# Optimization experiments

Hardware: AMD Instinct MI355X
Metric: run time of the kernel (lower is better)

Reference implementation:

```python
import jax, jax.numpy as jnp
import numpy as np

DEPTH = 4
DIM = 768
HEADS = 12
DH = 64
INNER = HEADS * DH            # 768
FF_INNER = int(4 * (2.0 / 3.0) * DIM)  # 2048 (GEGLU paper sizing)
B, N = 4, 1024                # N must be a perfect square (2D rotary)
ATTN_SCALE = 8.0              # cosine-sim attention scale from Attention(scale=8)
EPS = 1e-5


def _ln(x, gamma, beta):
    mu = jnp.mean(x, axis=-1, keepdims=True)
    var = jnp.mean((x - mu) ** 2, axis=-1, keepdims=True)
    return (x - mu) * jax.lax.rsqrt(var + EPS) * gamma + beta


def _rope_angles(n, dh):
    # precompute_freqs_cis_2d: x/y positions on sqrt(n) grid, dh//4 freqs each, interleaved
    H = int(n ** 0.5)
    pos = jnp.arange(n)
    xp = (pos % H).astype(jnp.float32)
    yp = (pos // H).astype(jnp.float32)
    freqs = 1.0 / (10000.0 ** (jnp.arange(0, dh, 4)[: dh // 4].astype(jnp.float32) / dh))
    xa = jnp.outer(xp, freqs)  # [n, dh//4]
    ya = jnp.outer(yp, freqs)
    return jnp.stack([xa, ya], axis=-1).reshape(n, dh // 2)  # [n, dh//2]


def _apply_rope(t, cos, sin):
    # t: [B, N, H, DH]; complex-pair rotation on last dim
    tr = t.reshape(*t.shape[:-1], DH // 2, 2)
    r, im = tr[..., 0], tr[..., 1]
    c = cos[None, :, None, :]
    s = sin[None, :, None, :]
    out = jnp.stack([r * c - im * s, r * s + im * c], axis=-1)
    return out.reshape(t.shape)


def _l2norm(t):
    return t / jnp.maximum(jnp.linalg.norm(t, axis=-1, keepdims=True), 1e-12)


def setup_inputs() -> dict:
    key = jax.random.key(0)
    ks = jax.random.split(key, 10)
    w = 0.02
    return {
        "x": jax.random.normal(ks[0], (B, N, DIM), dtype=jnp.float32),
        "attn_gamma": jnp.ones((DEPTH, DIM), dtype=jnp.float32),
        "wq": w * jax.random.normal(ks[1], (DEPTH, DIM, INNER), dtype=jnp.float32),
        "wkv": w * jax.random.normal(ks[2], (DEPTH, DIM, 2 * INNER), dtype=jnp.float32),
        "q_scale": jnp.ones((DEPTH, DH), dtype=jnp.float32),
        "k_scale": jnp.ones((DEPTH, DH), dtype=jnp.float32),
        "wo": w * jax.random.normal(ks[3], (DEPTH, INNER, DIM), dtype=jnp.float32),
        "ff_gamma": jnp.ones((DEPTH, DIM), dtype=jnp.float32),
        "ff_beta": jnp.zeros((DEPTH, DIM), dtype=jnp.float32),
        "wff1": w * jax.random.normal(ks[4], (DEPTH, DIM, 2 * FF_INNER), dtype=jnp.float32),
        "wff2": w * jax.random.normal(ks[5], (DEPTH, FF_INNER, DIM), dtype=jnp.float32),
    }


def reference(x, attn_gamma, wq, wkv, q_scale, k_scale, wo, ff_gamma, ff_beta, wff1, wff2):
    b, n, _ = x.shape
    ang = _rope_angles(n, DH)
    cos, sin = jnp.cos(ang), jnp.sin(ang)
    for i in range(DEPTH):
        # ---- Attention (qk-l2norm cosine attention, 2D rotary, scale=8) ----
        h = _ln(x, attn_gamma[i], 0.0)          # Attention.norm (beta is a zero buffer)
        kv_in = x                                # faithful: kv_input taken BEFORE norm
        q = (h @ wq[i]).reshape(b, n, HEADS, DH)
        kv = kv_in @ wkv[i]
        k, v = jnp.split(kv, 2, axis=-1)
        k = k.reshape(b, n, HEADS, DH)
        v = v.reshape(b, n, HEADS, DH)
        q = _apply_rope(q, cos, sin)
        k = _apply_rope(k, cos, sin)
        q = jnp.transpose(q, (0, 2, 1, 3))       # b h n d
        k = jnp.transpose(k, (0, 2, 1, 3))
        v = jnp.transpose(v, (0, 2, 1, 3))
        q = _l2norm(q) * q_scale[i]
        k = _l2norm(k) * k_scale[i]
        sim = jnp.einsum('bhid,bhjd->bhij', q, k) * ATTN_SCALE
        attn = jax.nn.softmax(sim, axis=-1)
        o = jnp.einsum('bhij,bhjd->bhid', attn, v)
        o = jnp.transpose(o, (0, 2, 1, 3)).reshape(b, n, INNER)
        x = x + o @ wo[i]
        # ---- GEGLU FeedForward ----
        hf = _ln(x, ff_gamma[i], ff_beta[i])
        u = hf @ wff1[i]
        a, g = jnp.split(u, 2, axis=-1)
        x = x + (a * jax.nn.gelu(g, approximate=False)) @ wff2[i]
    return x
```

## Files before the change

kernel.cpp:

```cpp
#include <hip/hip_runtime.h>
#include <hip/hip_bf16.h>
#include <math.h>

typedef __hip_bfloat16 bf16;
typedef __bf16 bf16x8 __attribute__((ext_vector_type(8)));
typedef float f32x4 __attribute__((ext_vector_type(4)));

#define NDEPTH 4
#define DIM 768
#define HEADS 12
#define DH 64
#define INNER 768
#define FFI 2048
#define BB 4
#define NN 1024
#define ROWS (BB*NN)

__device__ __forceinline__ void async_cp16(const bf16* g, bf16* l) {
  __builtin_amdgcn_global_load_lds(
      (const __attribute__((address_space(1))) unsigned int*)g,
      (__attribute__((address_space(3))) unsigned int*)l, 16, 0, 0);
}

template<int BN, bool GELU, bool VOUT, int K, int LD>
__device__ __forceinline__ void gemm_body(
    const bf16* __restrict__ A, const bf16* __restrict__ Bt,
    bf16* __restrict__ Cb, float* __restrict__ Cf, const float* __restrict__ Rf,
    bf16* __restrict__ Vt, int M, int N, int bx, int by, bf16* As, bf16* Bs)
{
  constexpr int WN = BN / 2;
  constexpr int NT = WN / 16;
  const int tid  = threadIdx.x;
  const int lane = tid & 63, w = tid >> 6;
  const int quad = lane >> 4, l16 = lane & 15;
  const int wr = w >> 1, wc = w & 1;
  const int m0 = by * 128, n0 = bx * BN;

  f32x4 acc[4][NT] = {};

  constexpr int CHA = 128 * 8;
  constexpr int CH  = CHA + BN * 8;
  constexpr int NCH = CH / 256;
  constexpr int NTK = K / 64;

  auto stage = [&](int kk, int buf) {
    bf16* Asb = As + buf * (128*64);
    bf16* Bsb = Bs + buf * (BN*64);
    #pragma unroll
    for (int t = 0; t < NCH; ++t) {
      int c0 = w*64 + t*256;
      int ch = c0 + lane;
      if (c0 < CHA) {
        int r = ch >> 3, j = (ch & 7) ^ (r & 7);
        async_cp16(&A[(size_t)(m0 + r)*LD + kk + j*8], &Asb[(size_t)c0*8]);
      } else {
        int ch2 = ch - CHA, r = ch2 >> 3, j = (ch2 & 7) ^ (r & 7);
        async_cp16(&Bt[(size_t)(n0 + r)*LD + kk + j*8], &Bsb[(size_t)(c0 - CHA)*8]);
      }
    }
  };

  stage(0, 0);
  __syncthreads();

  #pragma unroll
  for (int t = 0; t < NTK; ++t) {
    const int buf = t & 1;
    if (t + 1 < NTK) stage((t + 1) * 64, buf ^ 1);

    const bf16* Asb = As + buf * (128*64);
    const bf16* Bsb = Bs + buf * (BN*64);

    #pragma unroll
    for (int kc = 0; kc < 2; ++kc) {
      bf16x8 bfr[NT];
      #pragma unroll
      for (int nt = 0; nt < NT; ++nt) {
        int rb = wc*WN + nt*16 + l16;
        int c  = (kc*4 + quad) ^ (rb & 7);
        bfr[nt] = *(const bf16x8*)&Bsb[rb*64 + c*8];
      }
      #pragma unroll
      for (int mt = 0; mt < 4; ++mt) {
        int ra = wr*64 + mt*16 + l16;
        int ca = (kc*4 + quad) ^ (ra & 7);
        bf16x8 af = *(const bf16x8*)&Asb[ra*64 + ca*8];
        #pragma unroll
        for (int nt = 0; nt < NT; ++nt)
          acc[mt][nt] = __builtin_amdgcn_mfma_f32_16x16x32_bf16(af, bfr[nt], acc[mt][nt], 0, 0, 0);
      }
    }
    if (t + 1 < NTK) __syncthreads();
  }

  #pragma unroll
  for (int mt = 0; mt < 4; ++mt) {
    #pragma unroll
    for (int nt = 0; nt < NT; ++nt) {
      int row = m0 + wr*64 + mt*16 + quad*4;
      int col = n0 + wc*WN + nt*16 + l16;
      if (GELU) {
        #pragma unroll
        for (int r = 0; r < 4; ++r) {
          float v = acc[mt][nt][r];
          float g = __shfl_xor(v, 1);
          if (!(lane & 1)) {
            float ge = 0.5f * g * (1.f + erff(g * 0.70710678118654752f));
            Cb[(size_t)(row + r)*(N >> 1) + (col >> 1)] = __float2bfloat16(v * ge);
          }
        }
      } else if (VOUT) {
        if (col < INNER) {
          #pragma unroll
          for (int r = 0; r < 4; ++r)
            Cb[(size_t)(row + r)*INNER + col] = __float2bfloat16(acc[mt][nt][r]);
        } else {
          int c2 = col - INNER, hh = c2 >> 6, d = c2 & 63;
          int b = row >> 10, nn = row & 1023;
          union { ushort4 u4; bf16 h4[4]; } p;
          #pragma unroll
          for (int r = 0; r < 4; ++r) p.h4[r] = __float2bfloat16(acc[mt][nt][r]);
          *(ushort4*)&Vt[(((size_t)b*HEADS + hh)*DH + d)*NN + nn] = p.u4;
        }
      } else {
        #pragma unroll
        for (int r = 0; r < 4; ++r) {
          float v = acc[mt][nt][r];
          size_t idx = (size_t)(row + r) * N + col;
          if (Rf) v += Rf[idx];
          if (Cf) Cf[idx] = v;
          if (Cb) Cb[idx] = __float2bfloat16(v);
        }
      }
    }
  }
}

template<int BN, int KH, int LD>
__global__ __launch_bounds__(256) void gemm_splitk_kernel(
    const bf16* __restrict__ A, const bf16* __restrict__ Bt,
    float* __restrict__ P, int M, int N)
{
  __shared__ __align__(16) bf16 As[2*128*64];
  __shared__ __align__(16) bf16 Bs[2*BN*64];
  const int z = blockIdx.z;
  gemm_body<BN,false,false,KH,LD>(A + (size_t)z*KH, Bt + (size_t)z*KH, nullptr,
                                  P + (size_t)z*M*N, nullptr, nullptr,
                                  M, N, blockIdx.x, blockIdx.y, As, Bs);
}

__global__ __launch_bounds__(256) void qkv_kernel(
    const bf16* __restrict__ h, const bf16* __restrict__ x16,
    const bf16* __restrict__ wqT, const bf16* __restrict__ wkvT,
    bf16* __restrict__ qb, bf16* __restrict__ kb, bf16* __restrict__ vt)
{
  __shared__ __align__(16) bf16 As[2*128*64];
  __shared__ __align__(16) bf16 Bs[2*128*64];
  if (blockIdx.z == 0)
    gemm_body<64,false,false,768,768>(h, wqT, qb, nullptr, nullptr, nullptr,
                                      ROWS, INNER, blockIdx.x, blockIdx.y, As, Bs);
  else
    gemm_body<128,false,true,768,768>(x16, wkvT, kb, nullptr, nullptr, vt,
                                      ROWS, 2*INNER, blockIdx.x, blockIdx.y, As, Bs);
}

__global__ __launch_bounds__(512) void gemm256_kernel(
    const bf16* __restrict__ A, const bf16* __restrict__ Bt,
    bf16* __restrict__ Cb, int M, int N)
{
  __shared__ __align__(16) bf16 As[2][256*64];
  __shared__ __align__(16) bf16 Bs[2][256*64];

  const int tid  = threadIdx.x;
  const int lane = tid & 63, wv = tid >> 6;
  const int quad = lane >> 4, l16 = lane & 15;
  const int wr = wv >> 2, wc = wv & 3;

  const int lin = blockIdx.y * gridDim.x + blockIdx.x;
  const int xcd = lin & 7, loc = lin >> 3;
  const int bxs = (xcd & 1) * 8 + (loc & 7);
  const int bys = (xcd >> 1) * 4 + (loc >> 3);
  const int m0 = bys * 256, n0 = bxs * 256;

  f32x4 acc[8][4] = {};

  auto stage = [&](int kk, int buf) {
    #pragma unroll
    for (int t = 0; t < 8; ++t) {
      int c0 = wv*64 + t*512;
      int ch = c0 + lane;
      if (c0 < 2048) {
        int r = ch >> 3, j = (ch & 7) ^ (r & 7);
        async_cp16(&A[(size_t)(m0 + r)*768 + kk + j*8], &As[buf][(size_t)c0*8]);
      } else {
        int ch2 = ch - 2048, r = ch2 >> 3, j = (ch2 & 7) ^ (r & 7);
        async_cp16(&Bt[(size_t)(n0 + r)*768 + kk + j*8], &Bs[buf][(size_t)(c0 - 2048)*8]);
      }
    }
  };

  stage(0, 0);
  __syncthreads();

  #pragma unroll
  for (int t = 0; t < 12; ++t) {
    const int buf = t & 1;
    if (t + 1 < 12) stage((t + 1) * 64, buf ^ 1);

    const bf16* Asb = &As[buf][0];
    const bf16* Bsb = &Bs[buf][0];

    #pragma unroll
    for (int kc = 0; kc < 2; ++kc) {
      bf16x8 bfr[4];
      #pragma unroll
      for (int nt = 0; nt < 4; ++nt) {
        int rb = wc*64 + nt*16 + l16;
        int c  = (kc*4 + quad) ^ (rb & 7);
        bfr[nt] = *(const bf16x8*)&Bsb[rb*64 + c*8];
      }
      #pragma unroll
      for (int mt = 0; mt < 8; ++mt) {
        int ra = wr*128 + mt*16 + l16;
        int ca = (kc*4 + quad) ^ (ra & 7);
        bf16x8 af = *(const bf16x8*)&Asb[ra*64 + ca*8];
        #pragma unroll
        for (int nt = 0; nt < 4; ++nt)
          acc[mt][nt] = __builtin_amdgcn_mfma_f32_16x16x32_bf16(af, bfr[nt], acc[mt][nt], 0, 0, 0);
      }
    }
    if (t + 1 < 12) __syncthreads();
  }

  #pragma unroll
  for (int mt = 0; mt < 8; ++mt) {
    #pragma unroll
    for (int nt = 0; nt < 4; ++nt) {
      int row = m0 + wr*128 + mt*16 + quad*4;
      int col = n0 + wc*64 + nt*16 + l16;
      #pragma unroll
      for (int r = 0; r < 4; ++r) {
        float v = acc[mt][nt][r];
        float g = __shfl_xor(v, 1);
        if (!(lane & 1)) {
          float ge = 0.5f * g * (1.f + erff(g * 0.70710678118654752f));
          Cb[(size_t)(row + r)*(N >> 1) + (col >> 1)] = __float2bfloat16(v * ge);
        }
      }
    }
  }
}

__global__ __launch_bounds__(256) void ln_kernel(
    const float* __restrict__ x, const float* __restrict__ g,
    const float* __restrict__ bta, bf16* __restrict__ out)
{
  const int row = blockIdx.x, tid = threadIdx.x;
  const size_t base = (size_t)row * DIM;
  float v[3];
  #pragma unroll
  for (int j = 0; j < 3; ++j) v[j] = x[base + tid + j*256];
  float s  = v[0] + v[1] + v[2];
  float ss = v[0]*v[0] + v[1]*v[1] + v[2]*v[2];
  #pragma unroll
  for (int off = 32; off; off >>= 1) { s += __shfl_xor(s, off); ss += __shfl_xor(ss, off); }
  __shared__ float red[8];
  int w = tid >> 6;
  if ((tid & 63) == 0) { red[w] = s; red[w + 4] = ss; }
  __syncthreads();
  s  = red[0] + red[1] + red[2] + red[3];
  ss = red[4] + red[5] + red[6] + red[7];
  float mean = s * (1.f/768.f);
  float var  = ss * (1.f/768.f) - mean*mean;
  float rstd = rsqrtf(fmaxf(var, 0.f) + 1e-5f);
  #pragma unroll
  for (int j = 0; j < 3; ++j) {
    int c = tid + j*256;
    float bv = bta ? bta[c] : 0.f;
    out[base + c] = __float2bfloat16((v[j] - mean) * rstd * g[c] + bv);
  }
}

__global__ __launch_bounds__(256) void redln_kernel(
    const float* __restrict__ P0, const float* __restrict__ P1,
    const float* __restrict__ res,
    float* __restrict__ xo32, bf16* __restrict__ xo16, float* __restrict__ outf,
    const float* __restrict__ g, const float* __restrict__ bta,
    bf16* __restrict__ lnout)
{
  const int row = blockIdx.x, tid = threadIdx.x;
  const size_t base = (size_t)row * DIM;
  float v[3];
  #pragma unroll
  for (int j = 0; j < 3; ++j) {
    size_t idx = base + tid + j*256;
    v[j] = res[idx] + P0[idx] + P1[idx];
    if (xo32) xo32[idx] = v[j];
    if (xo16) xo16[idx] = __float2bfloat16(v[j]);
    if (outf) outf[idx] = v[j];
  }
  if (!g) return;
  float s  = v[0] + v[1] + v[2];
  float ss = v[0]*v[0] + v[1]*v[1] + v[2]*v[2];
  #pragma unroll
  for (int off = 32; off; off >>= 1) { s += __shfl_xor(s, off); ss += __shfl_xor(ss, off); }
  __shared__ float red[8];
  int w = tid >> 6;
  if ((tid & 63) == 0) { red[w] = s; red[w + 4] = ss; }
  __syncthreads();
  s  = red[0] + red[1] + red[2] + red[3];
  ss = red[4] + red[5] + red[6] + red[7];
  float mean = s * (1.f/768.f);
  float var  = ss * (1.f/768.f) - mean*mean;
  float rstd = rsqrtf(fmaxf(var, 0.f) + 1e-5f);
  #pragma unroll
  for (int j = 0; j < 3; ++j) {
    int c = tid + j*256;
    float bv = bta ? bta[c] : 0.f;
    lnout[base + c] = __float2bfloat16((v[j] - mean) * rstd * g[c] + bv);
  }
}

__global__ __launch_bounds__(384) void rope_kernel(
    const bf16* __restrict__ q, const bf16* __restrict__ kb,
    const float* __restrict__ qsc, const float* __restrict__ ksc,
    bf16* __restrict__ qh, bf16* __restrict__ kh)
{
  const int bn = blockIdx.x;
  const int b = bn >> 10, n = bn & 1023;
  const int tid = threadIdx.x;
  const int h = tid >> 5, pr = tid & 31, d0 = pr*2;
  const float xp = (float)(n & 31), yp = (float)(n >> 5);
  const int t = pr >> 1;
  const float freq = powf(10000.f, -(float)t / 16.f);
  const float ang = (pr & 1) ? yp * freq : xp * freq;
  float sn, cs;
  sincosf(ang, &sn, &cs);
  const float2 qs2 = *(const float2*)&qsc[d0];
  const float2 ks2 = *(const float2*)&ksc[d0];

  union { unsigned int u; bf16 h2[2]; } qa, ka, qo, ko;
  qa.u = *(const unsigned int*)&q [(size_t)bn*INNER + h*64 + d0];
  ka.u = *(const unsigned int*)&kb[(size_t)bn*INNER + h*64 + d0];
  float qre = __bfloat162float(qa.h2[0]), qim = __bfloat162float(qa.h2[1]);
  float kre = __bfloat162float(ka.h2[0]), kim = __bfloat162float(ka.h2[1]);
  float qr = qre*cs - qim*sn, qi = qre*sn + qim*cs;
  float kr = kre*cs - kim*sn, ki = kre*sn + kim*cs;
  float q2 = qr*qr + qi*qi, k2 = kr*kr + ki*ki;
  #pragma unroll
  for (int off = 1; off < 32; off <<= 1) { q2 += __shfl_xor(q2, off); k2 += __shfl_xor(k2, off); }
  float qinv = 8.f / fmaxf(sqrtf(q2), 1e-12f);
  float kinv = 1.f / fmaxf(sqrtf(k2), 1e-12f);
  qo.h2[0] = __float2bfloat16(qr * qinv * qs2.x);
  qo.h2[1] = __float2bfloat16(qi * qinv * qs2.y);
  ko.h2[0] = __float2bfloat16(kr * kinv * ks2.x);
  ko.h2[1] = __float2bfloat16(ki * kinv * ks2.y);
  size_t oi = (((size_t)b*HEADS + h)*NN + n)*DH + d0;
  *(unsigned int*)&qh[oi] = qo.u;
  *(unsigned int*)&kh[oi] = ko.u;
}

__global__ __launch_bounds__(256) void attn_kernel(
    const bf16* __restrict__ qh, const bf16* __restrict__ kh,
    const bf16* __restrict__ vt, const float* __restrict__ qsc,
    const float* __restrict__ ksc, bf16* __restrict__ ob)
{
  __shared__ __align__(16) bf16 Qs[64*64];
  __shared__ __align__(16) bf16 Ks[2][64*64];
  __shared__ __align__(16) bf16 Vs[2][64*64];
  __shared__ __align__(16) bf16 Ps[4][16*72];

  const int tid = threadIdx.x;
  const int lane = tid & 63, w = tid >> 6;
  const int quad = lane >> 4, l16 = lane & 15;
  const int qt = blockIdx.x, bh = blockIdx.y;
  const int b = bh / HEADS, h = bh % HEADS;
  const size_t base = (size_t)bh * NN * DH;

  float mq = fabsf(qsc[lane]), mk = fabsf(ksc[lane]);
  #pragma unroll
  for (int off = 1; off < 64; off <<= 1) {
    mq = fmaxf(mq, __shfl_xor(mq, off));
    mk = fmaxf(mk, __shfl_xor(mk, off));
  }
  const float Mb = 8.f * mq * mk;

  #pragma unroll
  for (int t = 0; t < 2; ++t) {
    int c0 = w*64 + t*256, ch = c0 + lane;
    int r = ch >> 3, jl = (ch & 7) ^ (r & 7);
    async_cp16(&qh[base + (size_t)(qt*64 + r)*64 + jl*8], &Qs[(size_t)c0*8]);
  }

  auto stage_kv = [&](int kt0, int buf) {
    #pragma unroll
    for (int t = 0; t < 4; ++t) {
      int c0 = w*64 + t*256, ch = c0 + lane;
      if (c0 < 512) {
        int r = ch >> 3, jl = (ch & 7) ^ (r & 7);
        async_cp16(&kh[base + (size_t)(kt0*64 + r)*64 + jl*8],
                   &Ks[buf][(size_t)c0*8]);
      } else {
        int ch2 = ch - 512, r = ch2 >> 3, jl = (ch2 & 7) ^ (r & 7);
        async_cp16(&vt[base + (size_t)r*NN + kt0*64 + jl*8],
                   &Vs[buf][(size_t)(c0 - 512)*8]);
      }
    }
  };

  f32x4 o[4] = {};
  float pl[4] = {0.f, 0.f, 0.f, 0.f};

  stage_kv(0, 0);
  __syncthreads();

  for (int kt0 = 0; kt0 < NN/64; ++kt0) {
    const int buf = kt0 & 1;
    if (kt0 + 1 < NN/64) stage_kv(kt0 + 1, buf ^ 1);

    f32x4 s[4] = {};
    bf16x8 aq[2];
    const int rq = w*16 + l16;
    #pragma unroll
    for (int kc = 0; kc < 2; ++kc)
      aq[kc] = *(const bf16x8*)&Qs[rq*64 + ((kc*4 + quad) ^ (rq & 7))*8];
    #pragma unroll
    for (int kt = 0; kt < 4; ++kt)
      #pragma unroll
      for (int kc = 0; kc < 2; ++kc) {
        int rb = kt*16 + l16;
        bf16x8 bk = *(const bf16x8*)&Ks[buf][rb*64 + ((kc*4 + quad) ^ (rb & 7))*8];
        s[kt] = __builtin_amdgcn_mfma_f32_16x16x32_bf16(aq[kc], bk, s[kt], 0, 0, 0);
      }

    #pragma unroll
    for (int r = 0; r < 4; ++r) {
      #pragma unroll
      for (int kt = 0; kt < 4; ++kt) {
        float pv = __expf(s[kt][r] - Mb);
        pl[r] += pv;
        Ps[w][(quad*4 + r)*72 + kt*16 + l16] = __float2bfloat16(pv);
      }
    }

    #pragma unroll
    for (int kc = 0; kc < 2; ++kc) {
      bf16x8 ap = *(const bf16x8*)&Ps[w][l16*72 + kc*32 + quad*8];
      #pragma unroll
      for (int nt = 0; nt < 4; ++nt) {
        int rv = nt*16 + l16;
        bf16x8 bv = *(const bf16x8*)&Vs[buf][rv*64 + ((kc*4 + quad) ^ (rv & 7))*8];
        o[nt] = __builtin_amdgcn_mfma_f32_16x16x32_bf16(ap, bv, o[nt], 0, 0, 0);
      }
    }

    if (kt0 + 1 < NN/64) __syncthreads();
  }

  float l[4];
  #pragma unroll
  for (int r = 0; r < 4; ++r) {
    float rs = pl[r];
    #pragma unroll
    for (int off = 1; off < 16; off <<= 1) rs += __shfl_xor(rs, off);
    l[r] = rs;
  }

  #pragma unroll
  for (int nt = 0; nt < 4; ++nt)
    #pragma unroll
    for (int r = 0; r < 4; ++r) {
      int n = qt*64 + w*16 + quad*4 + r;
      int dcol = nt*16 + l16;
      ob[((size_t)(b*NN + n)*HEADS + h)*DH + dcol] = __float2bfloat16(o[nt][r] / l[r]);
    }
}

__global__ __launch_bounds__(256) void cast_kernel(
    const float* __restrict__ x, bf16* __restrict__ o)
{
  size_t i = ((size_t)blockIdx.x*256 + threadIdx.x) * 8;
  float4 f0 = *(const float4*)(x + i);
  float4 f1 = *(const float4*)(x + i + 4);
  union { uint4 u; bf16 h[8]; } p;
  p.h[0] = __float2bfloat16(f0.x); p.h[1] = __float2bfloat16(f0.y);
  p.h[2] = __float2bfloat16(f0.z); p.h[3] = __float2bfloat16(f0.w);
  p.h[4] = __float2bfloat16(f1.x); p.h[5] = __float2bfloat16(f1.y);
  p.h[6] = __float2bfloat16(f1.z); p.h[7] = __float2bfloat16(f1.w);
  *(uint4*)(o + i) = p.u;
}

struct TD { const float* src; bf16* dst; int R, C, base, perm; };
struct TDs5 { TD d[5]; };

__global__ __launch_bounds__(256) void wtrans_kernel(TDs5 a)
{
  const int blk = blockIdx.x;
  int di = 0;
  #pragma unroll
  for (int k = 1; k < 5; ++k) if (blk >= a.d[k].base) di = k;
  const TD d = a.d[di];
  const int local = blk - d.base;
  const int tilesX = d.C >> 5;
  const int by = local / tilesX, bx = local - by*tilesX;
  __shared__ float t[32][33];
  const int tx = threadIdx.x & 31, ty = threadIdx.x >> 5;
  const int c0 = bx*32, r0 = by*32;
  #pragma unroll
  for (int i = 0; i < 4; ++i)
    t[ty + i*8][tx] = d.src[(size_t)(r0 + ty + i*8)*d.C + c0 + tx];
  __syncthreads();
  const int half = d.C >> 1;
  #pragma unroll
  for (int i = 0; i < 4; ++i) {
    int c = c0 + ty + i*8;
    int rout = d.perm ? ((c < half) ? 2*c : 2*(c - half) + 1) : c;
    d.dst[(size_t)rout*d.R + r0 + tx] = __float2bfloat16(t[tx][ty + i*8]);
  }
}

extern "C" void kernel_launch(void* const* d_in, const int* in_sizes, int n_in,
                              void* d_out, int out_size, void* d_ws, size_t ws_size,
                              hipStream_t stream)
{
  const float* x_in       = (const float*)d_in[0];
  const float* attn_gamma = (const float*)d_in[1];
  const float* wq         = (const float*)d_in[2];
  const float* wkv        = (const float*)d_in[3];
  const float* q_scale    = (const float*)d_in[4];
  const float* k_scale    = (const float*)d_in[5];
  const float* wo         = (const float*)d_in[6];
  const float* ff_gamma   = (const float*)d_in[7];
  const float* ff_beta    = (const float*)d_in[8];
  const float* wff1       = (const float*)d_in[9];
  const float* wff2       = (const float*)d_in[10];
  float* outp = (float*)d_out;
  char* ws = (char*)d_ws;

  const size_t E = (size_t)ROWS * DIM;
  float* xw32 = (float*)ws;
  bf16*  xw16 = (bf16*)(ws + 12582912);
  bf16*  S_h  = (bf16*)(ws + 18874368);
  char*  BIGb = ws + 25165824;
  bf16*  WT   = (bf16*)(ws + 62914560);
  bf16*  qbuf  = (bf16*)BIGb;
  bf16*  kbuf  = qbuf + E;
  bf16*  qhb   = qbuf + 2*E;
  bf16*  khb   = qbuf + 3*E;
  bf16*  vtb   = qbuf + 4*E;
  bf16*  glbuf = (bf16*)BIGb;
  float* wP    = (float*)BIGb;
  float* fP    = (float*)(BIGb + 16777216);
  bf16*  wqT   = WT;
  bf16*  wkvT  = WT + 589824;
  bf16*  woT   = WT + 1769472;
  bf16*  wff1T = WT + 2359296;
  bf16*  wff2T = WT + 5505024;

  cast_kernel<<<1536, 256, 0, stream>>>(x_in, xw16);
  ln_kernel<<<ROWS, 256, 0, stream>>>(x_in, attn_gamma, nullptr, S_h);

  for (int i = 0; i < NDEPTH; ++i) {
    const float* xsrc = (i == 0) ? x_in : xw32;

    TDs5 td;
    td.d[0] = { wq   + (size_t)i*589824,  wqT,   768,  768,    0, 0 };
    td.d[1] = { wkv  + (size_t)i*1179648, wkvT,  768, 1536,  576, 0 };
    td.d[2] = { wo   + (size_t)i*589824,  woT,   768,  768, 1728, 0 };
    td.d[3] = { wff1 + (size_t)i*3145728, wff1T, 768, 4096, 2304, 1 };
    td.d[4] = { wff2 + (size_t)i*1572864, wff2T, 2048, 768, 5376, 0 };
    wtrans_kernel<<<6912, 256, 0, stream>>>(td);

    qkv_kernel<<<dim3(12,32,2), 256, 0, stream>>>(S_h, xw16, wqT, wkvT, qbuf, kbuf, vtb);
    rope_kernel<<<ROWS, 384, 0, stream>>>(qbuf, kbuf, q_scale + i*DH, k_scale + i*DH, qhb, khb);
    attn_kernel<<<dim3(16,48), 256, 0, stream>>>(qhb, khb, vtb,
                                                 q_scale + i*DH, k_scale + i*DH, S_h);
    gemm_splitk_kernel<64,384,768><<<dim3(12,32,2), 256, 0, stream>>>(S_h, woT, wP, ROWS, DIM);
    redln_kernel<<<ROWS, 256, 0, stream>>>(wP, wP + E, xsrc, xw32, nullptr, nullptr,
                                           ff_gamma + i*DIM, ff_beta + i*DIM, S_h);
    gemm256_kernel<<<dim3(16,16), 512, 0, stream>>>(S_h, wff1T, glbuf, ROWS, 2*FFI);
    gemm_splitk_kernel<64,1024,2048><<<dim3(12,32,2), 256, 0, stream>>>(glbuf, wff2T, fP, ROWS, DIM);
    if (i < NDEPTH-1)
      redln_kernel<<<ROWS, 256, 0, stream>>>(fP, fP + E, xw32, xw32, xw16, nullptr,
                                             attn_gamma + (i+1)*DIM, nullptr, S_h);
    else
      redln_kernel<<<ROWS, 256, 0, stream>>>(fP, fP + E, xw32, nullptr, nullptr, outp,
                                             nullptr, nullptr, nullptr);
  }
}
```

Measured before the change: 907.9 us.

## Split 256x256 GEGLU GEMM K-tiles into half-stages with fine-grained async pipelining

Restructures the FF1 GEGLU GEMM main loop so each 64-wide K tile is split into two 32-wide halves with separate LDS buffers. Loads for A and B halves are issued interleaved with four MFMA phases, using partial vmcnt waits, raw s_barrier and s_setprio around MFMA bursts. The aim is to overlap global-to-LDS copies with matrix math more finely and cut full-tile barrier stalls. It adds manual waitcnt bookkeeping that must match the number of outstanding loads, which is fragile.

```diff
diff --git a/kernel.cpp b/kernel.cpp
--- a/kernel.cpp
+++ b/kernel.cpp
@@ -168,8 +168,8 @@
     const bf16* __restrict__ A, const bf16* __restrict__ Bt,
     bf16* __restrict__ Cb, int M, int N)
 {
-  __shared__ __align__(16) bf16 As[2][256*64];
-  __shared__ __align__(16) bf16 Bs[2][256*64];
+  __shared__ __align__(16) bf16 As[2][2][256*32];
+  __shared__ __align__(16) bf16 Bs[2][2][256*32];
 
   const int tid  = threadIdx.x;
   const int lane = tid & 63, wv = tid >> 6;
@@ -184,52 +184,96 @@
 
   f32x4 acc[8][4] = {};
 
-  auto stage = [&](int kk, int buf) {
-    #pragma unroll
-    for (int t = 0; t < 8; ++t) {
+  auto stage_half = [&](const bf16* __restrict__ G, int row0, int colbase,
+                        bf16* L) {
+    #pragma unroll
+    for (int t = 0; t < 2; ++t) {
       int c0 = wv*64 + t*512;
       int ch = c0 + lane;
-      if (c0 < 2048) {
-        int r = ch >> 3, j = (ch & 7) ^ (r & 7);
-        async_cp16(&A[(size_t)(m0 + r)*768 + kk + j*8], &As[buf][(size_t)c0*8]);
-      } else {
-        int ch2 = ch - 2048, r = ch2 >> 3, j = (ch2 & 7) ^ (r & 7);
-        async_cp16(&Bt[(size_t)(n0 + r)*768 + kk + j*8], &Bs[buf][(size_t)(c0 - 2048)*8]);
-      }
+      int r = ch >> 2, jsw = ch & 3, jh = jsw ^ (r & 3);
+      async_cp16(&G[(size_t)(row0 + r)*768 + colbase + jh*8],
+                 &L[(size_t)c0*8]);
     }
   };
 
-  stage(0, 0);
-  __syncthreads();
-
-  #pragma unroll
-  for (int t = 0; t < 12; ++t) {
-    const int buf = t & 1;
-    if (t + 1 < 12) stage((t + 1) * 64, buf ^ 1);
-
-    const bf16* Asb = &As[buf][0];
-    const bf16* Bsb = &Bs[buf][0];
-
-    #pragma unroll
-    for (int kc = 0; kc < 2; ++kc) {
-      bf16x8 bfr[4];
-      #pragma unroll
-      for (int nt = 0; nt < 4; ++nt) {
-        int rb = wc*64 + nt*16 + l16;
-        int c  = (kc*4 + quad) ^ (rb & 7);
-        bfr[nt] = *(const bf16x8*)&Bsb[rb*64 + c*8];
-      }
-      #pragma unroll
-      for (int mt = 0; mt < 8; ++mt) {
-        int ra = wr*128 + mt*16 + l16;
-        int ca = (kc*4 + quad) ^ (ra & 7);
-        bf16x8 af = *(const bf16x8*)&Asb[ra*64 + ca*8];
-        #pragma unroll
-        for (int nt = 0; nt < 4; ++nt)
-          acc[mt][nt] = __builtin_amdgcn_mfma_f32_16x16x32_bf16(af, bfr[nt], acc[mt][nt], 0, 0, 0);
-      }
-    }
-    if (t + 1 < 12) __syncthreads();
+  auto rdA = [&](const bf16* Ab, bf16x8* af) {
+    #pragma unroll
+    for (int mt = 0; mt < 8; ++mt) {
+      int ra = wr*128 + mt*16 + l16;
+      af[mt] = *(const bf16x8*)&Ab[ra*32 + (quad ^ (ra & 3))*8];
+    }
+  };
+  auto rdB = [&](const bf16* Bb, int ntg, bf16x8* bfr) {
+    #pragma unroll
+    for (int i = 0; i < 2; ++i) {
+      int rb = wc*64 + (ntg*2 + i)*16 + l16;
+      bfr[i] = *(const bf16x8*)&Bb[rb*32 + (quad ^ (rb & 3))*8];
+    }
+  };
+
+  stage_half(A,  m0, 0,  &As[0][0][0]);
+  stage_half(Bt, n0, 0,  &Bs[0][0][0]);
+  stage_half(A,  m0, 32, &As[0][1][0]);
+  stage_half(Bt, n0, 32, &Bs[0][1][0]);
+  asm volatile("s_waitcnt vmcnt(4)" ::: "memory");
+  __builtin_amdgcn_s_barrier();
+
+  #pragma unroll
+  for (int T = 0; T < 12; ++T) {
+    const int cur = T & 1, nxt = cur ^ 1;
+    const bf16 *A0 = &As[cur][0][0], *A1 = &As[cur][1][0];
+    const bf16 *B0 = &Bs[cur][0][0], *B1 = &Bs[cur][1][0];
+    const int kk1 = (T + 1) * 64;
+    bf16x8 af[8], bfr[2];
+
+    if (T + 1 < 12) stage_half(A, m0, kk1, &As[nxt][0][0]);
+    rdA(A0, af); rdB(B0, 0, bfr);
+    __builtin_amdgcn_s_setprio(1);
+    #pragma unroll
+    for (int mt = 0; mt < 8; ++mt)
+      #pragma unroll
+      for (int i = 0; i < 2; ++i)
+        acc[mt][i] = __builtin_amdgcn_mfma_f32_16x16x32_bf16(af[mt], bfr[i], acc[mt][i], 0, 0, 0);
+    __builtin_amdgcn_s_setprio(0);
+    __builtin_amdgcn_s_barrier();
+
+    if (T + 1 < 12) stage_half(Bt, n0, kk1, &Bs[nxt][0][0]);
+    rdB(B0, 1, bfr);
+    __builtin_amdgcn_s_setprio(1);
+    #pragma unroll
+    for (int mt = 0; mt < 8; ++mt)
+      #pragma unroll
+      for (int i = 0; i < 2; ++i)
+        acc[mt][2+i] = __builtin_amdgcn_mfma_f32_16x16x32_bf16(af[mt], bfr[i], acc[mt][2+i], 0, 0, 0);
+    __builtin_amdgcn_s_setprio(0);
+    if (T == 11) asm volatile("s_waitcnt vmcnt(0)" ::: "memory");
+    else         asm volatile("s_waitcnt vmcnt(4)" ::: "memory");
+    __builtin_amdgcn_s_barrier();
+
+    if (T + 1 < 12) stage_half(A, m0, kk1 + 32, &As[nxt][1][0]);
+    rdA(A1, af); rdB(B1, 0, bfr);
+    __builtin_amdgcn_s_setprio(1);
+    #pragma unroll
+    for (int mt = 0; mt < 8; ++mt)
+      #pragma unroll
+      for (int i = 0; i < 2; ++i)
+        acc[mt][i] = __builtin_amdgcn_mfma_f32_16x16x32_bf16(af[mt], bfr[i], acc[mt][i], 0, 0, 0);
+    __builtin_amdgcn_s_setprio(0);
+    __builtin_amdgcn_s_barrier();
+
+    if (T + 1 < 12) stage_half(Bt, n0, kk1 + 32, &Bs[nxt][1][0]);
+    rdB(B1, 1, bfr);
+    __builtin_amdgcn_s_setprio(1);
+    #pragma unroll
+    for (int mt = 0; mt < 8; ++mt)
+      #pragma unroll
+      for (int i = 0; i < 2; ++i)
+        acc[mt][2+i] = __builtin_amdgcn_mfma_f32_16x16x32_bf16(af[mt], bfr[i], acc[mt][2+i], 0, 0, 0);
+    __builtin_amdgcn_s_setprio(0);
+    if (T < 11) {
+      asm volatile("s_waitcnt vmcnt(4)" ::: "memory");
+      __builtin_amdgcn_s_barrier();
+    }
   }
 
   #pragma unroll
```

Result: no change. 913.7 us (+0.6%).
